# Performance work log

Measured on AMD Instinct MI355X. Metric: run time of the kernel, lower is better.

Reference implementation:

```python
import jax, jax.numpy as jnp
import numpy as np

MAX_LEN = 64  # global max_len in the original code


def _lstm_cell(h, c, x_t, Wih, Whh, bih, bhh):
    # torch LSTM gate order: i, f, g, o ; Wih/Whh are [4H, H]
    gates = x_t @ Wih.T + h @ Whh.T + bih + bhh  # [B, 4H]
    i, f, g, o = jnp.split(gates, 4, axis=-1)
    c_new = jax.nn.sigmoid(f) * c + jax.nn.sigmoid(i) * jnp.tanh(g)
    h_new = jax.nn.sigmoid(o) * jnp.tanh(c_new)
    return h_new, c_new


def setup_inputs() -> dict:
    V, H, B, S = 32000, 512, 32, 64
    key = jax.random.key(0)
    ks = jax.random.split(key, 12)
    sc_x = 1.0 / np.sqrt(H)
    inp = {
        "x": jax.random.randint(ks[0], (B, S), 0, V, dtype=jnp.int32),
        "emb": jax.random.normal(ks[1], (V, H), dtype=jnp.float32) * 0.02,
        "enc_Wih": jax.random.normal(ks[2], (4 * H, H), dtype=jnp.float32) * sc_x,
        "enc_Whh": jax.random.normal(ks[3], (4 * H, H), dtype=jnp.float32) * sc_x,
        "enc_bih": jnp.zeros((4 * H,), dtype=jnp.float32),
        "enc_bhh": jnp.zeros((4 * H,), dtype=jnp.float32),
        "dec_Wih": jax.random.normal(ks[4], (4 * H, H), dtype=jnp.float32) * sc_x,
        "dec_Whh": jax.random.normal(ks[5], (4 * H, H), dtype=jnp.float32) * sc_x,
        "dec_bih": jnp.zeros((4 * H,), dtype=jnp.float32),
        "dec_bhh": jnp.zeros((4 * H,), dtype=jnp.float32),
        "W_out": jax.random.normal(ks[6], (V, H), dtype=jnp.float32) * sc_x,
        "b_out": jnp.zeros((V,), dtype=jnp.float32),
        "dec_sos": 1,
    }
    return inp


def reference(x, emb, enc_Wih, enc_Whh, enc_bih, enc_bhh,
              dec_Wih, dec_Whh, dec_bih, dec_bhh, W_out, b_out, dec_sos):
    B, S = x.shape
    H = emb.shape[1]

    # ----- Encoder: LSTM over [B, S, H] embedded input -----
    x_emb = emb[x]  # [B, S, H]

    def enc_step(carry, e_t):
        h, c = carry
        h, c = _lstm_cell(h, c, e_t, enc_Wih, enc_Whh, enc_bih, enc_bhh)
        return (h, c), h

    h0 = jnp.zeros((B, H), dtype=emb.dtype)
    c0 = jnp.zeros((B, H), dtype=emb.dtype)
    (h_enc, c_enc), enc_out = jax.lax.scan(enc_step, (h0, c0),
                                           jnp.swapaxes(x_emb, 0, 1))
    enc_out = jnp.swapaxes(enc_out, 0, 1)  # [B, S, H]

    # ----- Greedy decode loop: emb -> LSTM step -> linear -> log_softmax -> argmax -----
    tok0 = jnp.full((B,), dec_sos, dtype=x.dtype)

    def dec_step(carry, _):
        h, c, tok = carry
        e = emb[tok]  # [B, H]
        h, c = _lstm_cell(h, c, e, dec_Wih, dec_Whh, dec_bih, dec_bhh)
        logp = jax.nn.log_softmax(h @ W_out.T + b_out, axis=-1)  # [B, V]
        nxt = jnp.argmax(logp, axis=-1).astype(x.dtype)  # topk(1) index
        return (h, c, nxt), (nxt, logp)

    (_, _, _), (toks, logps) = jax.lax.scan(
        dec_step, (h_enc, c_enc, tok0), None, length=MAX_LEN)

    out1 = jnp.swapaxes(toks, 0, 1)   # [B, MAX_LEN] greedy token ids
    out2 = jnp.swapaxes(logps, 0, 1)  # [B, MAX_LEN, V] log-probs (squeezed)
    return out1, out2, enc_out
```

## Files before the change

kernel.cpp:

```cpp
#include <hip/hip_runtime.h>
#include <math.h>

#define VOC 32000
#define HID 512
#define BAT 32
#define SEQ 64

#define B_EIHT 0u
#define B_EHHT 4194304u
#define B_DIHT 8388608u
#define B_DHHT 12582912u
#define B_XD   16777216u
#define B_H    33554432u
#define B_C    33685504u
#define B_E    33816576u
#define B_GT   33882112u
#define B_LG   34144256u
#define B_PM   38240256u
#define B_PS   38305792u
#define B_PK   38371328u
#define B_M    38502400u
#define B_LS   38502528u
#define B_TK   38502656u

#define OUT_TOK  0u
#define OUT_LOGP 2048u
#define OUT_ENC  65538048u

__device__ __forceinline__ unsigned long long packkey(float x, int v) {
    unsigned int fb = __float_as_uint(x);
    unsigned int key = (fb & 0x80000000u) ? ~fb : (fb | 0x80000000u);
    return ((unsigned long long)key << 32) | (unsigned int)(~(unsigned int)v);
}
__device__ __forceinline__ float sigf(float x) { return 1.0f / (1.0f + expf(-x)); }

__global__ void k_tr(const float* __restrict__ src, float* __restrict__ dst) {
    __shared__ float lds[32][33];
    int c0 = blockIdx.x * 32, r0 = blockIdx.y * 32;
    int cl = threadIdx.x & 31, r8 = threadIdx.x >> 5;
    for (int rr = 0; rr < 4; ++rr) {
        int r = r8 + rr * 8;
        lds[r][cl] = src[(size_t)(r0 + r) * HID + c0 + cl];
    }
    __syncthreads();
    for (int rr = 0; rr < 4; ++rr) {
        int idx = threadIdx.x + rr * 256;
        int rl = idx & 31, c2 = idx >> 5;
        dst[(size_t)(c0 + c2) * 2048 + r0 + rl] = lds[rl][c2];
    }
}

__global__ void k_zero(char* __restrict__ ws) {
    int i = blockIdx.x * 256 + threadIdx.x;
    ((float*)(ws + B_H))[i] = 0.f;
    ((float*)(ws + B_C))[i] = 0.f;
}

__global__ void __launch_bounds__(256) k_xd(const int* __restrict__ x, const float* __restrict__ emb,
                                            char* __restrict__ ws) {
    __shared__ float e_s[512];
    int r = blockIdx.x;
    int j4 = blockIdx.y * 256 + threadIdx.x;
    const float* erow = emb + (size_t)x[r] * HID;
    for (int k = threadIdx.x; k < HID; k += 256) e_s[k] = erow[k];
    __syncthreads();
    const float* WT = (const float*)(ws + B_EIHT);
    float acc = 0.f;
    for (int k = 0; k < HID; ++k)
        acc = fmaf(WT[(size_t)k * 2048 + j4], e_s[k], acc);
    ((float*)(ws + B_XD))[(size_t)r * 2048 + j4] = acc;
}

__global__ void __launch_bounds__(256) k_gates(const float* __restrict__ bih,
                                               const float* __restrict__ bhh,
                                               const float* __restrict__ Hin,
                                               char* __restrict__ ws, int t, int mode) {
    __shared__ float h_s[512];
    __shared__ float e_s[512];
    int b = blockIdx.x & 31, jb = blockIdx.x >> 5;
    int j4 = jb * 256 + threadIdx.x;
    for (int k = threadIdx.x; k < HID; k += 256) {
        h_s[k] = Hin[b * HID + k];
        if (mode == 1) e_s[k] = ((const float*)(ws + B_E))[b * HID + k];
    }
    __syncthreads();
    float xd;
    if (mode == 0) {
        xd = ((const float*)(ws + B_XD))[(size_t)(b * SEQ + t) * 2048 + j4];
    } else {
        const float* WT = (const float*)(ws + B_DIHT);
        float a = 0.f;
        for (int k = 0; k < HID; ++k)
            a = fmaf(WT[(size_t)k * 2048 + j4], e_s[k], a);
        xd = a;
    }
    const float* WH = (const float*)(ws + (mode == 0 ? B_EHHT : B_DHHT));
    float hd = 0.f;
    for (int k = 0; k < HID; ++k)
        hd = fmaf(WH[(size_t)k * 2048 + j4], h_s[k], hd);
    float g = (xd + hd) + bih[j4];
    g = g + bhh[j4];
    ((float*)(ws + B_GT))[b * 2048 + j4] = g;
}

__global__ void k_cell(char* __restrict__ ws,
                       const float* __restrict__ Cin,
                       float* __restrict__ Hout, float* __restrict__ Cout,
                       float* __restrict__ dout, int t, int mode) {
    int i = blockIdx.x * 256 + threadIdx.x;
    int b = i >> 9, j = i & 511;
    const float* gb = (const float*)(ws + B_GT) + b * 2048;
    float ip = sigf(gb[j]);
    float fp = sigf(gb[512 + j]);
    float gp = tanhf(gb[1024 + j]);
    float op = sigf(gb[1536 + j]);
    float cn = fp * Cin[i] + ip * gp;
    float hn = op * tanhf(cn);
    Hout[i] = hn;
    Cout[i] = cn;
    if (mode == 0)
        dout[OUT_ENC + (size_t)b * (SEQ * HID) + (size_t)t * HID + j] = hn;
}

__global__ void k_embt(const int* __restrict__ sos, const float* __restrict__ emb,
                       char* __restrict__ ws, int t) {
    int b = blockIdx.x;
    int tok = (t == 0) ? sos[0] : ((const int*)(ws + B_TK))[b];
    const float* erow = emb + (size_t)tok * HID;
    for (int k = threadIdx.x; k < HID; k += 256)
        ((float*)(ws + B_E))[b * HID + k] = erow[k];
}

__global__ void __launch_bounds__(256) k_logits(const float* __restrict__ Hin,
                                                const float* __restrict__ Wout,
                                                const float* __restrict__ bout,
                                                char* __restrict__ ws) {
    __shared__ float h2[16][512];
    int vb = blockIdx.x, bh = blockIdx.y;
    for (int i = threadIdx.x; i < 16 * 512; i += 256) {
        int bb = i >> 9, k = i & 511;
        h2[bb][k] = Hin[(bh * 16 + bb) * HID + k];
    }
    __syncthreads();
    int v = vb * 256 + threadIdx.x;
    const float* wr = Wout + (size_t)v * HID;
    float acc[16];
#pragma unroll
    for (int i = 0; i < 16; ++i) acc[i] = 0.f;
    for (int k = 0; k < HID; k += 4) {
        float4 w = *(const float4*)&wr[k];
#pragma unroll
        for (int bb = 0; bb < 16; ++bb) {
            float4 h4 = *(const float4*)&h2[bb][k];
            float a = acc[bb];
            a = fmaf(w.x, h4.x, a);
            a = fmaf(w.y, h4.y, a);
            a = fmaf(w.z, h4.z, a);
            a = fmaf(w.w, h4.w, a);
            acc[bb] = a;
        }
    }
    float bq = bout[v];
    float mx[16];
#pragma unroll
    for (int bb = 0; bb < 16; ++bb) {
        float lg = acc[bb] + bq;
        ((float*)(ws + B_LG))[(size_t)(bh * 16 + bb) * VOC + v] = lg;
        mx[bb] = lg;
    }
#pragma unroll
    for (int m = 1; m < 64; m <<= 1)
#pragma unroll
        for (int bb = 0; bb < 16; ++bb) mx[bb] = fmaxf(mx[bb], __shfl_xor(mx[bb], m));
    if ((threadIdx.x & 63) == 0) {
        int col = vb * 4 + (threadIdx.x >> 6);
#pragma unroll
        for (int bb = 0; bb < 16; ++bb)
            ((float*)(ws + B_PM))[(bh * 16 + bb) * 512 + col] = mx[bb];
    }
}

__global__ void k_finM(char* __restrict__ ws) {
    __shared__ float sh[4];
    int b = blockIdx.x;
    float m = -3.4e38f;
    for (int c = threadIdx.x; c < 500; c += 256)
        m = fmaxf(m, ((const float*)(ws + B_PM))[b * 512 + c]);
#pragma unroll
    for (int k = 1; k < 64; k <<= 1) m = fmaxf(m, __shfl_xor(m, k));
    if ((threadIdx.x & 63) == 0) sh[threadIdx.x >> 6] = m;
    __syncthreads();
    if (threadIdx.x == 0)
        ((float*)(ws + B_M))[b] = fmaxf(fmaxf(sh[0], sh[1]), fmaxf(sh[2], sh[3]));
}

__global__ void __launch_bounds__(256) k_passB(char* __restrict__ ws) {
    int vb = blockIdx.x, bg = blockIdx.y;
    int b0 = bg * 2;
    int v = vb * 256 + threadIdx.x;
    float e2[2];
#pragma unroll
    for (int row = 0; row < 2; ++row) {
        int b = b0 + row;
        float m = ((const float*)(ws + B_M))[b];
        float* p = (float*)(ws + B_LG) + (size_t)b * VOC + v;
        float sv = *p - m;
        *p = sv;
        e2[row] = expf(sv);
    }
#pragma unroll
    for (int m = 1; m < 64; m <<= 1) {
        e2[0] += __shfl_xor(e2[0], m);
        e2[1] += __shfl_xor(e2[1], m);
    }
    if ((threadIdx.x & 63) == 0) {
        int col = vb * 4 + (threadIdx.x >> 6);
        ((float*)(ws + B_PS))[b0 * 512 + col] = e2[0];
        ((float*)(ws + B_PS))[(b0 + 1) * 512 + col] = e2[1];
    }
}

__global__ void k_finS(char* __restrict__ ws) {
    __shared__ float sh[4];
    int b = blockIdx.x;
    float s = 0.f;
    for (int c = threadIdx.x; c < 500; c += 256)
        s += ((const float*)(ws + B_PS))[b * 512 + c];
#pragma unroll
    for (int k = 1; k < 64; k <<= 1) s += __shfl_xor(s, k);
    if ((threadIdx.x & 63) == 0) sh[threadIdx.x >> 6] = s;
    __syncthreads();
    if (threadIdx.x == 0)
        ((float*)(ws + B_LS))[b] = logf(sh[0] + sh[1] + sh[2] + sh[3]);
}

__global__ void __launch_bounds__(256) k_passC(char* __restrict__ ws, float* __restrict__ dout, int t) {
    int vb = blockIdx.x, bg = blockIdx.y;
    int b0 = bg * 2;
    int v = vb * 256 + threadIdx.x;
    unsigned long long pk2[2];
#pragma unroll
    for (int row = 0; row < 2; ++row) {
        int b = b0 + row;
        float L = ((const float*)(ws + B_LS))[b];
        float sv = ((const float*)(ws + B_LG))[(size_t)b * VOC + v];
        float lp = sv - L;
        dout[OUT_LOGP + (size_t)(b * SEQ + t) * VOC + v] = lp;
        pk2[row] = packkey(lp, v);
    }
#pragma unroll
    for (int m = 1; m < 64; m <<= 1) {
#pragma unroll
        for (int row = 0; row < 2; ++row) {
            unsigned long long o = __shfl_xor(pk2[row], m);
            if (o > pk2[row]) pk2[row] = o;
        }
    }
    if ((threadIdx.x & 63) == 0) {
        int col = vb * 4 + (threadIdx.x >> 6);
        ((unsigned long long*)(ws + B_PK))[b0 * 512 + col] = pk2[0];
        ((unsigned long long*)(ws + B_PK))[(b0 + 1) * 512 + col] = pk2[1];
    }
}

__global__ void k_finT(char* __restrict__ ws, float* __restrict__ dout, int t) {
    __shared__ unsigned long long sh[4];
    int b = blockIdx.x;
    unsigned long long pk = 0ull;
    for (int c = threadIdx.x; c < 500; c += 256) {
        unsigned long long o = ((const unsigned long long*)(ws + B_PK))[b * 512 + c];
        if (o > pk) pk = o;
    }
#pragma unroll
    for (int k = 1; k < 64; k <<= 1) {
        unsigned long long o = __shfl_xor(pk, k);
        if (o > pk) pk = o;
    }
    if ((threadIdx.x & 63) == 0) sh[threadIdx.x >> 6] = pk;
    __syncthreads();
    if (threadIdx.x == 0) {
        pk = sh[0];
        if (sh[1] > pk) pk = sh[1];
        if (sh[2] > pk) pk = sh[2];
        if (sh[3] > pk) pk = sh[3];
        int v = (int)(~(unsigned)(pk & 0xFFFFFFFFull));
        ((int*)(ws + B_TK))[b] = v;
        dout[OUT_TOK + b * SEQ + t] = (float)v;
    }
}

extern "C" void kernel_launch(void* const* d_in, const int* in_sizes, int n_in,
                              void* d_out, int out_size, void* d_ws, size_t ws_size,
                              hipStream_t stream) {
    const int*   x    = (const int*)d_in[0];
    const float* emb  = (const float*)d_in[1];
    const float* eWih = (const float*)d_in[2];
    const float* eWhh = (const float*)d_in[3];
    const float* ebih = (const float*)d_in[4];
    const float* ebhh = (const float*)d_in[5];
    const float* dWih = (const float*)d_in[6];
    const float* dWhh = (const float*)d_in[7];
    const float* dbih = (const float*)d_in[8];
    const float* dbhh = (const float*)d_in[9];
    const float* Wout = (const float*)d_in[10];
    const float* bout = (const float*)d_in[11];
    const int*   sos  = (const int*)d_in[12];
    float* out = (float*)d_out;
    char*  ws  = (char*)d_ws;

    float* H = (float*)(ws + B_H);
    float* C = (float*)(ws + B_C);

    hipLaunchKernelGGL(k_tr, dim3(16, 64), dim3(256), 0, stream, eWih, (float*)(ws + B_EIHT));
    hipLaunchKernelGGL(k_tr, dim3(16, 64), dim3(256), 0, stream, eWhh, (float*)(ws + B_EHHT));
    hipLaunchKernelGGL(k_tr, dim3(16, 64), dim3(256), 0, stream, dWih, (float*)(ws + B_DIHT));
    hipLaunchKernelGGL(k_tr, dim3(16, 64), dim3(256), 0, stream, dWhh, (float*)(ws + B_DHHT));
    hipLaunchKernelGGL(k_xd, dim3(2048, 8), dim3(256), 0, stream, x, emb, ws);
    hipLaunchKernelGGL(k_zero, dim3(64), dim3(256), 0, stream, ws);

    for (int t = 0; t < SEQ; ++t) {
        int pi = t & 1, po = pi ^ 1;
        hipLaunchKernelGGL(k_gates, dim3(256), dim3(256), 0, stream,
                           ebih, ebhh, H + pi * 16384, ws, t, 0);
        hipLaunchKernelGGL(k_cell, dim3(64), dim3(256), 0, stream,
                           ws, C + pi * 16384, H + po * 16384, C + po * 16384, out, t, 0);
    }
    for (int t = 0; t < SEQ; ++t) {
        int pi = t & 1, po = pi ^ 1;
        hipLaunchKernelGGL(k_embt, dim3(32), dim3(256), 0, stream, sos, emb, ws, t);
        hipLaunchKernelGGL(k_gates, dim3(256), dim3(256), 0, stream,
                           dbih, dbhh, H + pi * 16384, ws, t, 1);
        hipLaunchKernelGGL(k_cell, dim3(64), dim3(256), 0, stream,
                           ws, C + pi * 16384, H + po * 16384, C + po * 16384, out, t, 1);
        hipLaunchKernelGGL(k_logits, dim3(125, 2), dim3(256), 0, stream,
                           H + po * 16384, Wout, bout, ws);
        hipLaunchKernelGGL(k_finM, dim3(32), dim3(256), 0, stream, ws);
        hipLaunchKernelGGL(k_passB, dim3(125, 16), dim3(256), 0, stream, ws);
        hipLaunchKernelGGL(k_finS, dim3(32), dim3(256), 0, stream, ws);
        hipLaunchKernelGGL(k_passC, dim3(125, 16), dim3(256), 0, stream, ws, out, t);
        hipLaunchKernelGGL(k_finT, dim3(32), dim3(256), 0, stream, ws, out, t);
    }
}
```

Before: 9.202 ms.

## Fuse small reduction and embedding kernels into neighbours to cut per-step launches

Removes the k_embt, k_finM, k_finS and k_finT launches per decode step. Their work moves into other kernels: the argmax finish and embedding gather go into k_gates, the max finalize is recomputed in every k_passB block, and the sum/log finalize in every k_passC block. The last token is written by one kernel after the loop. k_gates now reads h directly from global memory instead of LDS, and k_logits uses 8 batch rows per block with 4 y-blocks and reads h from global instead of shared memory. This cuts launch and serialization overhead, but each block repeats the small reductions redundantly.

```diff
diff --git a/kernel.cpp b/kernel.cpp
--- a/kernel.cpp
+++ b/kernel.cpp
@@ -13,15 +13,11 @@
 #define B_XD   16777216u
 #define B_H    33554432u
 #define B_C    33685504u
-#define B_E    33816576u
 #define B_GT   33882112u
 #define B_LG   34144256u
 #define B_PM   38240256u
 #define B_PS   38305792u
 #define B_PK   38371328u
-#define B_M    38502400u
-#define B_LS   38502528u
-#define B_TK   38502656u
 
 #define OUT_TOK  0u
 #define OUT_LOGP 2048u
@@ -73,34 +69,74 @@
 
 __global__ void __launch_bounds__(256) k_gates(const float* __restrict__ bih,
                                                const float* __restrict__ bhh,
+                                               const float* __restrict__ emb,
+                                               const int* __restrict__ sos,
                                                const float* __restrict__ Hin,
-                                               char* __restrict__ ws, int t, int mode) {
-    __shared__ float h_s[512];
+                                               char* __restrict__ ws,
+                                               float* __restrict__ dout,
+                                               int t, int mode) {
     __shared__ float e_s[512];
-    int b = blockIdx.x & 31, jb = blockIdx.x >> 5;
-    int j4 = jb * 256 + threadIdx.x;
-    for (int k = threadIdx.x; k < HID; k += 256) {
-        h_s[k] = Hin[b * HID + k];
-        if (mode == 1) e_s[k] = ((const float*)(ws + B_E))[b * HID + k];
-    }
-    __syncthreads();
-    float xd;
-    if (mode == 0) {
-        xd = ((const float*)(ws + B_XD))[(size_t)(b * SEQ + t) * 2048 + j4];
+    __shared__ unsigned long long psh[4];
+    __shared__ int toksh;
+    int b = blockIdx.x >> 3, jc = blockIdx.x & 7;
+    int j4 = jc * 256 + threadIdx.x;
+    const float* hb = Hin + b * HID;
+
+    if (mode == 1) {
+        int tok;
+        if (t == 0) {
+            tok = sos[0];
+        } else {
+            const unsigned long long* pkr = (const unsigned long long*)(ws + B_PK) + b * 512;
+            unsigned long long pk = 0ull;
+            for (int c = threadIdx.x; c < 500; c += 256) {
+                unsigned long long o = pkr[c];
+                if (o > pk) pk = o;
+            }
+#pragma unroll
+            for (int m = 1; m < 64; m <<= 1) {
+                unsigned long long o = __shfl_xor(pk, m);
+                if (o > pk) pk = o;
+            }
+            if ((threadIdx.x & 63) == 0) psh[threadIdx.x >> 6] = pk;
+            __syncthreads();
+            if (threadIdx.x == 0) {
+                pk = psh[0];
+                if (psh[1] > pk) pk = psh[1];
+                if (psh[2] > pk) pk = psh[2];
+                if (psh[3] > pk) pk = psh[3];
+                int v = (int)(~(unsigned)(pk & 0xFFFFFFFFull));
+                toksh = v;
+                if (jc == 0) dout[OUT_TOK + b * SEQ + (t - 1)] = (float)v;
+            }
+            __syncthreads();
+            tok = toksh;
+        }
+        const float* erow = emb + (size_t)tok * HID;
+        e_s[threadIdx.x] = erow[threadIdx.x];
+        e_s[threadIdx.x + 256] = erow[threadIdx.x + 256];
+        __syncthreads();
+
+        const float* WI = (const float*)(ws + B_DIHT);
+        const float* WH = (const float*)(ws + B_DHHT);
+        float aI = 0.f, aH = 0.f;
+        for (int k = 0; k < HID; ++k) {
+            aI = fmaf(WI[(size_t)k * 2048 + j4], e_s[k], aI);
+            aH = fmaf(WH[(size_t)k * 2048 + j4], hb[k], aH);
+        }
+        float g = (aI + aH) + bih[j4];
+        g = g + bhh[j4];
+        ((float*)(ws + B_GT))[b * 2048 + j4] = g;
     } else {
-        const float* WT = (const float*)(ws + B_DIHT);
-        float a = 0.f;
+        const float* WH = (const float*)(ws + B_EHHT);
+        float aH = 0.f;
         for (int k = 0; k < HID; ++k)
-            a = fmaf(WT[(size_t)k * 2048 + j4], e_s[k], a);
-        xd = a;
-    }
-    const float* WH = (const float*)(ws + (mode == 0 ? B_EHHT : B_DHHT));
-    float hd = 0.f;
-    for (int k = 0; k < HID; ++k)
-        hd = fmaf(WH[(size_t)k * 2048 + j4], h_s[k], hd);
-    float g = (xd + hd) + bih[j4];
-    g = g + bhh[j4];
-    ((float*)(ws + B_GT))[b * 2048 + j4] = g;
+            aH = fmaf(WH[(size_t)k * 2048 + j4], hb[k], aH);
+        float xd = ((const float*)(ws + B_XD))[(size_t)(b * SEQ + t) * 2048 + j4];
+        float g = (xd + aH) + bih[j4];
+        g = g + bhh[j4];
+        ((float*)(ws + B_GT))[b * 2048 + j4] = g;
+    }
 }
 
 __global__ void k_cell(char* __restrict__ ws,
@@ -122,36 +158,21 @@
         dout[OUT_ENC + (size_t)b * (SEQ * HID) + (size_t)t * HID + j] = hn;
 }
 
-__global__ void k_embt(const int* __restrict__ sos, const float* __restrict__ emb,
-                       char* __restrict__ ws, int t) {
-    int b = blockIdx.x;
-    int tok = (t == 0) ? sos[0] : ((const int*)(ws + B_TK))[b];
-    const float* erow = emb + (size_t)tok * HID;
-    for (int k = threadIdx.x; k < HID; k += 256)
-        ((float*)(ws + B_E))[b * HID + k] = erow[k];
-}
-
 __global__ void __launch_bounds__(256) k_logits(const float* __restrict__ Hin,
                                                 const float* __restrict__ Wout,
                                                 const float* __restrict__ bout,
                                                 char* __restrict__ ws) {
-    __shared__ float h2[16][512];
     int vb = blockIdx.x, bh = blockIdx.y;
-    for (int i = threadIdx.x; i < 16 * 512; i += 256) {
-        int bb = i >> 9, k = i & 511;
-        h2[bb][k] = Hin[(bh * 16 + bb) * HID + k];
-    }
-    __syncthreads();
     int v = vb * 256 + threadIdx.x;
     const float* wr = Wout + (size_t)v * HID;
-    float acc[16];
-#pragma unroll
-    for (int i = 0; i < 16; ++i) acc[i] = 0.f;
+    float acc[8];
+#pragma unroll
+    for (int i = 0; i < 8; ++i) acc[i] = 0.f;
     for (int k = 0; k < HID; k += 4) {
         float4 w = *(const float4*)&wr[k];
 #pragma unroll
-        for (int bb = 0; bb < 16; ++bb) {
-            float4 h4 = *(const float4*)&h2[bb][k];
+        for (int bb = 0; bb < 8; ++bb) {
+            float4 h4 = *(const float4*)&Hin[(size_t)(bh * 8 + bb) * HID + k];
             float a = acc[bb];
             a = fmaf(w.x, h4.x, a);
             a = fmaf(w.y, h4.y, a);
@@ -161,50 +182,57 @@
         }
     }
     float bq = bout[v];
-    float mx[16];
-#pragma unroll
-    for (int bb = 0; bb < 16; ++bb) {
+    float mx[8];
+#pragma unroll
+    for (int bb = 0; bb < 8; ++bb) {
         float lg = acc[bb] + bq;
-        ((float*)(ws + B_LG))[(size_t)(bh * 16 + bb) * VOC + v] = lg;
+        ((float*)(ws + B_LG))[(size_t)(bh * 8 + bb) * VOC + v] = lg;
         mx[bb] = lg;
     }
 #pragma unroll
     for (int m = 1; m < 64; m <<= 1)
 #pragma unroll
-        for (int bb = 0; bb < 16; ++bb) mx[bb] = fmaxf(mx[bb], __shfl_xor(mx[bb], m));
+        for (int bb = 0; bb < 8; ++bb) mx[bb] = fmaxf(mx[bb], __shfl_xor(mx[bb], m));
     if ((threadIdx.x & 63) == 0) {
         int col = vb * 4 + (threadIdx.x >> 6);
 #pragma unroll
-        for (int bb = 0; bb < 16; ++bb)
-            ((float*)(ws + B_PM))[(bh * 16 + bb) * 512 + col] = mx[bb];
-    }
-}
-
-__global__ void k_finM(char* __restrict__ ws) {
-    __shared__ float sh[4];
-    int b = blockIdx.x;
-    float m = -3.4e38f;
-    for (int c = threadIdx.x; c < 500; c += 256)
-        m = fmaxf(m, ((const float*)(ws + B_PM))[b * 512 + c]);
-#pragma unroll
-    for (int k = 1; k < 64; k <<= 1) m = fmaxf(m, __shfl_xor(m, k));
-    if ((threadIdx.x & 63) == 0) sh[threadIdx.x >> 6] = m;
-    __syncthreads();
-    if (threadIdx.x == 0)
-        ((float*)(ws + B_M))[b] = fmaxf(fmaxf(sh[0], sh[1]), fmaxf(sh[2], sh[3]));
+        for (int bb = 0; bb < 8; ++bb)
+            ((float*)(ws + B_PM))[(bh * 8 + bb) * 512 + col] = mx[bb];
+    }
 }
 
 __global__ void __launch_bounds__(256) k_passB(char* __restrict__ ws) {
+    __shared__ float msh[2][4];
     int vb = blockIdx.x, bg = blockIdx.y;
     int b0 = bg * 2;
     int v = vb * 256 + threadIdx.x;
+    float m0 = -3.4e38f, m1 = -3.4e38f;
+    const float* pm0 = (const float*)(ws + B_PM) + b0 * 512;
+    const float* pm1 = (const float*)(ws + B_PM) + (b0 + 1) * 512;
+    for (int c = threadIdx.x; c < 500; c += 256) {
+        m0 = fmaxf(m0, pm0[c]);
+        m1 = fmaxf(m1, pm1[c]);
+    }
+#pragma unroll
+    for (int k = 1; k < 64; k <<= 1) {
+        m0 = fmaxf(m0, __shfl_xor(m0, k));
+        m1 = fmaxf(m1, __shfl_xor(m1, k));
+    }
+    if ((threadIdx.x & 63) == 0) {
+        msh[0][threadIdx.x >> 6] = m0;
+        msh[1][threadIdx.x >> 6] = m1;
+    }
+    __syncthreads();
+    float M[2];
+    M[0] = fmaxf(fmaxf(msh[0][0], msh[0][1]), fmaxf(msh[0][2], msh[0][3]));
+    M[1] = fmaxf(fmaxf(msh[1][0], msh[1][1]), fmaxf(msh[1][2], msh[1][3]));
+
     float e2[2];
 #pragma unroll
     for (int row = 0; row < 2; ++row) {
         int b = b0 + row;
-        float m = ((const float*)(ws + B_M))[b];
         float* p = (float*)(ws + B_LG) + (size_t)b * VOC + v;
-        float sv = *p - m;
+        float sv = *p - M[row];
         *p = sv;
         e2[row] = expf(sv);
     }
@@ -220,31 +248,38 @@
     }
 }
 
-__global__ void k_finS(char* __restrict__ ws) {
-    __shared__ float sh[4];
-    int b = blockIdx.x;
-    float s = 0.f;
-    for (int c = threadIdx.x; c < 500; c += 256)
-        s += ((const float*)(ws + B_PS))[b * 512 + c];
-#pragma unroll
-    for (int k = 1; k < 64; k <<= 1) s += __shfl_xor(s, k);
-    if ((threadIdx.x & 63) == 0) sh[threadIdx.x >> 6] = s;
-    __syncthreads();
-    if (threadIdx.x == 0)
-        ((float*)(ws + B_LS))[b] = logf(sh[0] + sh[1] + sh[2] + sh[3]);
-}
-
 __global__ void __launch_bounds__(256) k_passC(char* __restrict__ ws, float* __restrict__ dout, int t) {
+    __shared__ float ssh0[4], ssh1[4];
     int vb = blockIdx.x, bg = blockIdx.y;
     int b0 = bg * 2;
     int v = vb * 256 + threadIdx.x;
+    const float* ps0 = (const float*)(ws + B_PS) + b0 * 512;
+    const float* ps1 = (const float*)(ws + B_PS) + (b0 + 1) * 512;
+    float s0 = 0.f, s1 = 0.f;
+    for (int c = threadIdx.x; c < 500; c += 256) {
+        s0 += ps0[c];
+        s1 += ps1[c];
+    }
+#pragma unroll
+    for (int k = 1; k < 64; k <<= 1) {
+        s0 += __shfl_xor(s0, k);
+        s1 += __shfl_xor(s1, k);
+    }
+    if ((threadIdx.x & 63) == 0) {
+        ssh0[threadIdx.x >> 6] = s0;
+        ssh1[threadIdx.x >> 6] = s1;
+    }
+    __syncthreads();
+    float L[2];
+    L[0] = logf(((ssh0[0] + ssh0[1]) + ssh0[2]) + ssh0[3]);
+    L[1] = logf(((ssh1[0] + ssh1[1]) + ssh1[2]) + ssh1[3]);
+
     unsigned long long pk2[2];
 #pragma unroll
     for (int row = 0; row < 2; ++row) {
         int b = b0 + row;
-        float L = ((const float*)(ws + B_LS))[b];
         float sv = ((const float*)(ws + B_LG))[(size_t)b * VOC + v];
-        float lp = sv - L;
+        float lp = sv - L[row];
         dout[OUT_LOGP + (size_t)(b * SEQ + t) * VOC + v] = lp;
         pk2[row] = packkey(lp, v);
     }
@@ -263,7 +298,7 @@
     }
 }
 
-__global__ void k_finT(char* __restrict__ ws, float* __restrict__ dout, int t) {
+__global__ void k_tokfin(char* __restrict__ ws, float* __restrict__ dout) {
     __shared__ unsigned long long sh[4];
     int b = blockIdx.x;
     unsigned long long pk = 0ull;
@@ -284,8 +319,7 @@
         if (sh[2] > pk) pk = sh[2];
         if (sh[3] > pk) pk = sh[3];
         int v = (int)(~(unsigned)(pk & 0xFFFFFFFFull));
-        ((int*)(ws + B_TK))[b] = v;
-        dout[OUT_TOK + b * SEQ + t] = (float)v;
+        dout[OUT_TOK + b * SEQ + 63] = (float)v;
     }
 }
 
@@ -321,23 +355,20 @@
     for (int t = 0; t < SEQ; ++t) {
         int pi = t & 1, po = pi ^ 1;
         hipLaunchKernelGGL(k_gates, dim3(256), dim3(256), 0, stream,
-                           ebih, ebhh, H + pi * 16384, ws, t, 0);
+                           ebih, ebhh, emb, sos, H + pi * 16384, ws, out, t, 0);
         hipLaunchKernelGGL(k_cell, dim3(64), dim3(256), 0, stream,
                            ws, C + pi * 16384, H + po * 16384, C + po * 16384, out, t, 0);
     }
     for (int t = 0; t < SEQ; ++t) {
         int pi = t & 1, po = pi ^ 1;
-        hipLaunchKernelGGL(k_embt, dim3(32), dim3(256), 0, stream, sos, emb, ws, t);
         hipLaunchKernelGGL(k_gates, dim3(256), dim3(256), 0, stream,
-                           dbih, dbhh, H + pi * 16384, ws, t, 1);
+                           dbih, dbhh, emb, sos, H + pi * 16384, ws, out, t, 1);
         hipLaunchKernelGGL(k_cell, dim3(64), dim3(256), 0, stream,
                            ws, C + pi * 16384, H + po * 16384, C + po * 16384, out, t, 1);
-        hipLaunchKernelGGL(k_logits, dim3(125, 2), dim3(256), 0, stream,
+        hipLaunchKernelGGL(k_logits, dim3(125, 4), dim3(256), 0, stream,
                            H + po * 16384, Wout, bout, ws);
-        hipLaunchKernelGGL(k_finM, dim3(32), dim3(256), 0, stream, ws);
         hipLaunchKernelGGL(k_passB, dim3(125, 16), dim3(256), 0, stream, ws);
-        hipLaunchKernelGGL(k_finS, dim3(32), dim3(256), 0, stream, ws);
         hipLaunchKernelGGL(k_passC, dim3(125, 16), dim3(256), 0, stream, ws, out, t);
-        hipLaunchKernelGGL(k_finT, dim3(32), dim3(256), 0, stream, ws, out, t);
-    }
-}
+    }
+    hipLaunchKernelGGL(k_tokfin, dim3(32), dim3(256), 0, stream, ws, out);
+}
```

Measured after the change: 8.866 ms. 3.7% less time.
